# Kernel tuning notes

Hardware: AMD Instinct MI355X
Metric: run time of the kernel (lower is better)

## Reference

```python
import jax, jax.numpy as jnp
import numpy as np

DIM = 256
CTX_DIM = 768
GROUPS = 8
EPS = 1e-5


def setup_inputs() -> dict:
    key = jax.random.key(0)
    ks = jax.random.split(key, 16)
    B, C, H, W, L = 16, DIM, 64, 64, 77
    s_conv = 1.0 / np.sqrt(C * 9)
    s_q = 1.0 / np.sqrt(C)
    s_kv = 1.0 / np.sqrt(CTX_DIM)
    return {
        "x": jax.random.normal(ks[0], (B, C, H, W), jnp.float32),
        "context": jax.random.normal(ks[1], (B, L, CTX_DIM), jnp.float32),
        "conv_w": jax.random.uniform(ks[2], (C, C, 3, 3), jnp.float32, -s_conv, s_conv),
        "conv_b": jax.random.uniform(ks[3], (C,), jnp.float32, -s_conv, s_conv),
        "gn_w": jnp.ones((C,), jnp.float32),
        "gn_b": jnp.zeros((C,), jnp.float32),
        "wq": jax.random.uniform(ks[4], (C, C), jnp.float32, -s_q, s_q),
        "bq": jax.random.uniform(ks[5], (C,), jnp.float32, -s_q, s_q),
        "wk": jax.random.uniform(ks[6], (C, CTX_DIM), jnp.float32, -s_kv, s_kv),
        "bk": jax.random.uniform(ks[7], (C,), jnp.float32, -s_kv, s_kv),
        "wv": jax.random.uniform(ks[8], (C, CTX_DIM), jnp.float32, -s_kv, s_kv),
        "bv": jax.random.uniform(ks[9], (C,), jnp.float32, -s_kv, s_kv),
        "wo": jax.random.uniform(ks[10], (C, C), jnp.float32, -s_q, s_q),
        "bo": jax.random.uniform(ks[11], (C,), jnp.float32, -s_q, s_q),
    }


def _group_norm(h, gn_w, gn_b):
    B, C, H, W = h.shape
    g = h.reshape(B, GROUPS, C // GROUPS, H, W)
    mean = g.mean(axis=(2, 3, 4), keepdims=True)
    var = g.var(axis=(2, 3, 4), keepdims=True)
    g = (g - mean) * jax.lax.rsqrt(var + EPS)
    h = g.reshape(B, C, H, W)
    return h * gn_w[None, :, None, None] + gn_b[None, :, None, None]


def reference(x, context, conv_w, conv_b, gn_w, gn_b, wq, bq, wk, bk, wv, bv, wo, bo):
    B, C, H, W = x.shape
    # conv 3x3, padding=1 (NCHW, OIHW)
    h = jax.lax.conv_general_dilated(
        x, conv_w, window_strides=(1, 1), padding=((1, 1), (1, 1)),
        dimension_numbers=("NCHW", "OIHW", "NCHW"))
    h = h + conv_b[None, :, None, None]
    h = jax.nn.silu(_group_norm(h, gn_w, gn_b))
    # flatten spatial -> tokens: [B, HW, C]
    hf = h.reshape(B, C, H * W).transpose(0, 2, 1)
    q = hf @ wq.T + bq                     # [B, HW, C]
    k = context @ wk.T + bk                # [B, L, C]
    v = context @ wv.T + bv                # [B, L, C]
    scale = 1.0 / jnp.sqrt(jnp.asarray(C, q.dtype))
    att = jax.nn.softmax(jnp.einsum("bqc,bkc->bqk", q, k) * scale, axis=-1)
    o = jnp.einsum("bqk,bkc->bqc", att, v) @ wo.T + bo
    h_att = o.transpose(0, 2, 1).reshape(B, C, H, W)
    return x + h_att
```

## Files before the change

### kernel.cpp

```cpp
#include <hip/hip_runtime.h>
#include <stdint.h>

#define B_  16
#define C_  256
#define HW_ 4096
#define Hp  66
#define PP  4356
#define EPS_ 1e-5f

typedef unsigned short u16;
typedef unsigned int   u32;
typedef __attribute__((ext_vector_type(4))) float  f32x4;
typedef __attribute__((ext_vector_type(8))) __bf16 bf16x8;
typedef __attribute__((ext_vector_type(8))) u16    u16x8;

__device__ __forceinline__ float bf2f(u16 u){ u32 x = ((u32)u)<<16; float f; __builtin_memcpy(&f,&x,4); return f; }
__device__ __forceinline__ u16 f2bf(float f){ u32 x; __builtin_memcpy(&x,&f,4); u32 r = x + 0x7fffu + ((x>>16)&1u); return (u16)(r>>16); }

__device__ __forceinline__ void g2l16(const void* g, void* l){
  __builtin_amdgcn_global_load_lds((__attribute__((address_space(1))) void*)(void*)g,
                                   (__attribute__((address_space(3))) void*)l, 16, 0, 0);
}
__device__ __forceinline__ bf16x8 ldfrag(const u16* p){
  u16x8 r = *(const u16x8*)p;
  return __builtin_bit_cast(bf16x8, r);
}

__global__ __launch_bounds__(256) void k_prep(const float* __restrict__ x, u16* __restrict__ xpT,
    const float* __restrict__ conv_w, const float* __restrict__ wq, const float* __restrict__ wo,
    const float* __restrict__ wk, const float* __restrict__ wv, const float* __restrict__ ctx,
    u16* __restrict__ wBt, u16* __restrict__ wqB, u16* __restrict__ woB,
    u16* __restrict__ wkvB, u16* __restrict__ ctxB, float* __restrict__ stats){
  __shared__ float Lt[64*65];
  int bid = blockIdx.x; int tid = threadIdx.x;
  if(bid >= 1056){
    int i = (bid-1056)*256 + tid;
    if(i < 589824){
      int j = i&7, co = (i>>3)&255, atom = (i>>11)&3, g = i>>13;
      int t = g%9, cic = g/9;
      int ciF = cic*32 + atom*8 + j;
      wBt[i] = f2bf(conv_w[(co*256+ciF)*9 + t]); return;
    }
    i -= 589824;
    if(i < 65536){ wqB[i] = f2bf(wq[i]); return; } i -= 65536;
    if(i < 65536){ woB[i] = f2bf(wo[i]); return; } i -= 65536;
    if(i < 196608){ wkvB[i] = f2bf(wk[i]); return; } i -= 196608;
    if(i < 196608){ wkvB[196608+i] = f2bf(wv[i]); return; } i -= 196608;
    if(i < 946176){ ctxB[i] = f2bf(ctx[i]); return; } i -= 946176;
    if(i < 512){ stats[i] = 0.f; }
    return;
  }
  int b = bid/66, hh = bid - b*66;
  if(hh==0 || hh==65){
    for(int i=tid;i<32*264;i+=256){
      int pl = i/264, off = i - pl*264;
      u32* p = (u32*)(xpT + ((size_t)(b*32+pl)*PP + (size_t)hh*Hp)*8);
      p[off] = 0u;
    }
    return;
  }
  {
    int pl = tid>>3, q = tid&7;
    size_t base = ((size_t)(b*32+pl)*PP + (size_t)hh*Hp + (q>=4?65:0))*8;
    ((u32*)(xpT + base))[q&3] = 0u;
  }
  int h = hh-1;
  for(int cc=0; cc<4; cc++){
    int c0=cc*64;
    int ci = tid>>2, w0 = (tid&3)*16;
    const float* xs = x + ((size_t)(b*C_ + c0+ci)*HW_) + h*64 + w0;
    for(int j=0;j<4;j++){
      float4 v = *(const float4*)(xs + j*4);
      Lt[ci*65 + w0 + j*4 + 0] = v.x;
      Lt[ci*65 + w0 + j*4 + 1] = v.y;
      Lt[ci*65 + w0 + j*4 + 2] = v.z;
      Lt[ci*65 + w0 + j*4 + 3] = v.w;
    }
    __syncthreads();
    int w = tid>>2, cj = (tid&3)*16;
    union { u16 u[16]; uint4 v[2]; } outu;
    for(int j=0;j<16;j++) outu.u[j] = f2bf(Lt[(cj+j)*65 + w]);
    int chan = c0 + cj;
    int cic = chan>>5, at0 = (chan>>3)&3;
    u16* dst = xpT + (((size_t)(b*8+cic)*4 + at0)*PP + (size_t)hh*Hp + w + 1)*8;
    *(uint4*)dst = outu.v[0];
    *(uint4*)(dst + (size_t)PP*8) = outu.v[1];
    __syncthreads();
  }
}

__global__ __launch_bounds__(256, 3) void k_conv(const u16* __restrict__ xpT, const u16* __restrict__ wBt,
    const float* __restrict__ conv_b, u16* __restrict__ h, float* __restrict__ stats){
  __shared__ u16 As[2][264*32];
  __shared__ u16 Bs[2][128*32];
  int bid0 = blockIdx.x;
  int l = (bid0 & 7)*128 + (bid0 >> 3);
  int b = l >> 6, hp = (l >> 1) & 31, nh = l & 1;
  int tid = threadIdx.x;
  int w = tid>>6, lane = tid&63, ln = lane&15, qd = lane>>4;
  int wm = w&1, wn = w>>1;
  f32x4 acc[4][4] = {};
  int hr_[4], wp_[4];
  #pragma unroll
  for(int mf=0;mf<4;mf++){ int p = wm*64 + mf*16 + ln; hr_[mf] = p>>6; wp_[mf] = p&63; }

  #pragma unroll
  for(int r=0;r<5;r++){
    int c = r*256 + tid;
    if(c < 1056){
      int atom = c/264, ipix = c - atom*264;
      g2l16(xpT + (((size_t)(b*8+0)*4 + atom)*PP + hp*132 + ipix)*8, &As[0][c*8]);
    }
  }
  #pragma unroll
  for(int r=0;r<2;r++){
    int c = r*256 + tid;
    int atom = c>>7, col = c&127;
    g2l16(wBt + ((size_t)atom*2048 + (nh*128+col)*8), &Bs[0][c*8]);
  }
  __syncthreads();

  int cb = 0;
  for(int ci=0; ci<8; ci++){
    int ca = ci&1;
    for(int t=0;t<9;t++){
      int tn = t+1, cin = ci;
      if(tn==9){ tn=0; cin=ci+1; }
      if(cin < 8){
        #pragma unroll
        for(int r=0;r<2;r++){
          int c = r*256 + tid;
          int atom = c>>7, col = c&127;
          g2l16(wBt + (((size_t)(cin*9+tn)*4 + atom)*2048 + (nh*128+col)*8), &Bs[cb^1][c*8]);
        }
      }
      if(t<5 && ci<7){
        int c = t*256 + tid;
        if(c < 1056){
          int atom = c/264, ipix = c - atom*264;
          g2l16(xpT + (((size_t)(b*8+ci+1)*4 + atom)*PP + hp*132 + ipix)*8, &As[ca^1][c*8]);
        }
      }
      int dy = (t*11)>>5, dx = t - dy*3;
      bf16x8 af[4], bfv[4];
      #pragma unroll
      for(int mf=0;mf<4;mf++){
        int ipix = (hr_[mf]+dy)*66 + wp_[mf] + dx;
        af[mf] = ldfrag(&As[ca][(qd*264 + ipix)*8]);
      }
      #pragma unroll
      for(int nf=0;nf<4;nf++) bfv[nf] = ldfrag(&Bs[cb][(qd*128 + wn*64+nf*16+ln)*8]);
      #pragma unroll
      for(int mf=0;mf<4;mf++)
        #pragma unroll
        for(int nf=0;nf<4;nf++)
          acc[mf][nf] = __builtin_amdgcn_mfma_f32_16x16x32_bf16(af[mf], bfv[nf], acc[mf][nf], 0,0,0);
      __syncthreads();
      cb ^= 1;
    }
  }
  float s[2]={0,0}, q[2]={0,0};
  int p0 = hp*128;
  for(int nf=0;nf<4;nf++){
    int n = nh*128 + wn*64 + nf*16 + ln;
    float bias = conv_b[n];
    for(int mf=0;mf<4;mf++){
      for(int r=0;r<4;r++){
        int p = wm*64 + mf*16 + qd*4 + r;
        float v = acc[mf][nf][r] + bias;
        h[((size_t)(b*HW_ + p0 + p))*C_ + n] = f2bf(v);
        s[nf>>1]+=v; q[nf>>1]+=v*v;
      }
    }
  }
  for(int off=32;off>=1;off>>=1){
    #pragma unroll
    for(int g=0;g<2;g++){ s[g]+=__shfl_down(s[g],off,64); q[g]+=__shfl_down(q[g],off,64); }
  }
  if(lane==0){
    #pragma unroll
    for(int g=0;g<2;g++){
      int gg = nh*4 + wn*2 + g;
      atomicAdd(&stats[(b*8 + gg)*2+0], s[g]);
      atomicAdd(&stats[(b*8 + gg)*2+1], q[g]);
    }
  }
}

__global__ __launch_bounds__(256, 2) void k_qgn(const u16* __restrict__ hbuf, const u16* __restrict__ wqB,
    const float* __restrict__ stats, const float* __restrict__ gnw, const float* __restrict__ gnb,
    const float* __restrict__ bq, u16* __restrict__ qb){
  __shared__ u16 As[128*32];
  __shared__ u16 Bs[256*32];
  int mt = blockIdx.x;
  int b = mt >> 5;
  int tid = threadIdx.x;
  int w = tid>>6, lane = tid&63, ln = lane&15, qd = lane>>4;
  int wm = w&1, wn = w>>1;
  int pr = tid>>1, half = tid&1;
  const u16* hsrc = hbuf + ((size_t)(mt*128+pr))*256 + half*16;
  f32x4 acc[4][8] = {};
  uint4 ra0, ra1, rb0, rb1;
  ra0 = *(const uint4*)(hsrc);
  ra1 = *(const uint4*)(hsrc + 8);
  for(int kt=0; kt<8; kt++){
    float sm = stats[(b*8+kt)*2], qm = stats[(b*8+kt)*2+1];
    float mean = sm*(1.f/131072.f);
    float rstd = rsqrtf(qm*(1.f/131072.f) - mean*mean + EPS_);
    int c0 = kt*32 + half*16;
    float4 gw0 = *(const float4*)(gnw+c0), gw1 = *(const float4*)(gnw+c0+4);
    float4 gw2 = *(const float4*)(gnw+c0+8), gw3 = *(const float4*)(gnw+c0+12);
    float4 gb0 = *(const float4*)(gnb+c0), gb1 = *(const float4*)(gnb+c0+4);
    float4 gb2 = *(const float4*)(gnb+c0+8), gb3 = *(const float4*)(gnb+c0+12);
    float gwv[16] = {gw0.x,gw0.y,gw0.z,gw0.w, gw1.x,gw1.y,gw1.z,gw1.w,
                     gw2.x,gw2.y,gw2.z,gw2.w, gw3.x,gw3.y,gw3.z,gw3.w};
    float gbv[16] = {gb0.x,gb0.y,gb0.z,gb0.w, gb1.x,gb1.y,gb1.z,gb1.w,
                     gb2.x,gb2.y,gb2.z,gb2.w, gb3.x,gb3.y,gb3.z,gb3.w};
    u16 inu[16];
    ((uint4*)inu)[0] = ra0; ((uint4*)inu)[1] = ra1;
    u16 outu[16];
    #pragma unroll
    for(int j=0;j<16;j++){
      float v = bf2f(inu[j]);
      v = (v-mean)*rstd*gwv[j] + gbv[j];
      float s = v/(1.f+__expf(-v));
      outu[j] = f2bf(s);
    }
    u16* adst = &As[pr*32 + half*16];
    ((uint4*)adst)[0] = ((uint4*)outu)[0];
    ((uint4*)adst)[1] = ((uint4*)outu)[1];
    #pragma unroll
    for(int r=0;r<4;r++){
      int c = r*256 + tid;
      int co = c>>2, atom = c&3;
      g2l16(wqB + (size_t)co*256 + kt*32 + atom*8, &Bs[c*8]);
    }
    if(kt<7){
      rb0 = *(const uint4*)(hsrc + (kt+1)*32);
      rb1 = *(const uint4*)(hsrc + (kt+1)*32 + 8);
    }
    __syncthreads();
    bf16x8 af[4], bfv[8];
    #pragma unroll
    for(int mf=0;mf<4;mf++) af[mf] = ldfrag(&As[(wm*64+mf*16+ln)*32 + qd*8]);
    #pragma unroll
    for(int nf=0;nf<8;nf++) bfv[nf] = ldfrag(&Bs[(wn*128+nf*16+ln)*32 + qd*8]);
    #pragma unroll
    for(int mf=0;mf<4;mf++)
      #pragma unroll
      for(int nf=0;nf<8;nf++)
        acc[mf][nf] = __builtin_amdgcn_mfma_f32_16x16x32_bf16(af[mf], bfv[nf], acc[mf][nf], 0,0,0);
    __syncthreads();
    ra0 = rb0; ra1 = rb1;
  }
  for(int nf=0;nf<8;nf++){
    int n = wn*128 + nf*16 + ln;
    float bias = bq[n];
    for(int mf=0;mf<4;mf++){
      for(int r=0;r<4;r++){
        int ml = wm*64 + mf*16 + qd*4 + r;
        qb[((size_t)(mt*128+ml))*256 + n] = f2bf(acc[mf][nf][r]+bias);
      }
    }
  }
}

__global__ __launch_bounds__(256) void k_kvproj(const u16* __restrict__ ctxB, const u16* __restrict__ wkvB,
    const float* __restrict__ bk, const float* __restrict__ bv,
    u16* __restrict__ kb, u16* __restrict__ vT){
  __shared__ u16 As[64*128];
  __shared__ u16 Bs[64*128];
  int bid = blockIdx.x;
  int nt = bid & 7, mt = bid >> 3;
  int n0 = nt*64, m0 = mt*64;
  int tid=threadIdx.x, w=tid>>6, lane=tid&63, ln=lane&15, qd=lane>>4;
  int wm = w&1, wn = w>>1;
  f32x4 acc[2][2]={};
  for(int kt=0;kt<6;kt++){
    #pragma unroll
    for(int r=0;r<4;r++){
      int c = r*256 + tid;
      int row = c>>4, atom = c&15;
      g2l16(ctxB + ((size_t)(m0+row)*768 + kt*128 + atom*8), &As[c*8]);
      g2l16(wkvB + ((size_t)(n0+row)*768 + kt*128 + atom*8), &Bs[c*8]);
    }
    __syncthreads();
    #pragma unroll
    for(int kk=0;kk<4;kk++){
      bf16x8 af[2], bfv[2];
      #pragma unroll
      for(int mf=0;mf<2;mf++) af[mf]=ldfrag(&As[(wm*32+mf*16+ln)*128 + kk*32 + qd*8]);
      #pragma unroll
      for(int nf=0;nf<2;nf++) bfv[nf]=ldfrag(&Bs[(wn*32+nf*16+ln)*128 + kk*32 + qd*8]);
      #pragma unroll
      for(int mf=0;mf<2;mf++)
        #pragma unroll
        for(int nf=0;nf<2;nf++)
          acc[mf][nf]=__builtin_amdgcn_mfma_f32_16x16x32_bf16(af[mf],bfv[nf],acc[mf][nf],0,0,0);
    }
    __syncthreads();
  }
  for(int mf=0;mf<2;mf++) for(int nf=0;nf<2;nf++){
    int ng = n0 + wn*32 + nf*16 + ln;
    float bias = ng<256 ? bk[ng] : bv[ng-256];
    for(int r=0;r<4;r++){
      int mg = m0 + wm*32 + mf*16 + qd*4 + r;
      if(mg<1232){
        float v=acc[mf][nf][r]+bias;
        int bb=mg/77, l=mg-bb*77;
        if(ng<256) kb[((size_t)(bb*77+l))*256+ng]=f2bf(v);
        else vT[((size_t)(bb*256+(ng-256)))*96 + l]=f2bf(v);
      }
    }
  }
}

__global__ __launch_bounds__(256) void k_attn(const u16* __restrict__ qg, const u16* __restrict__ kb,
    const u16* __restrict__ vT, u16* __restrict__ ob){
  __shared__ u16 Qs[4096];
  __shared__ u16 KVs[4096];
  __shared__ u16 Sb[128*88];
  __shared__ u16 Pb[128*104];
  __shared__ float invr[128];
  int bid=blockIdx.x; int b=bid>>5, qt=bid&31; int p0=qt*128;
  int tid=threadIdx.x, w=tid>>6, lane=tid&63, ln=lane&15, qd=lane>>4;
  int srow=tid>>2, koff=(tid&3)*8;
  f32x4 Sa[2][5]={};
  for(int kt=0;kt<8;kt++){
    for(int j=0;j<2;j++){
      int m=srow+j*64;
      g2l16(qg + ((size_t)(b*HW_+p0+m)*256 + kt*32+koff), &Qs[(size_t)tid*8+j*2048]);
    }
    for(int j=0;j<2;j++){
      int cja = tid + j*256;
      if(cja < 320){
        int l = cja>>2, ko2=(cja&3)*8;
        g2l16(kb + ((size_t)(b*77+l)*256 + kt*32+ko2), &KVs[(size_t)cja*8]);
      }
    }
    __syncthreads();
    bf16x8 af[2], bfv[5];
    for(int mf=0;mf<2;mf++) af[mf]=ldfrag(&Qs[(w*32+mf*16+ln)*32+qd*8]);
    for(int nf=0;nf<5;nf++) bfv[nf]=ldfrag(&KVs[(nf*16+ln)*32+qd*8]);
    for(int mf=0;mf<2;mf++) for(int nf=0;nf<5;nf++)
      Sa[mf][nf]=__builtin_amdgcn_mfma_f32_16x16x32_bf16(af[mf],bfv[nf],Sa[mf][nf],0,0,0);
    __syncthreads();
  }
  for(int mf=0;mf<2;mf++) for(int nf=0;nf<5;nf++) for(int r=0;r<4;r++){
    int ml=w*32+mf*16+qd*4+r, nl=nf*16+ln;
    Sb[ml*88+nl]=f2bf(Sa[mf][nf][r]*0.0625f);
  }
  __syncthreads();
  if(tid<128){
    u16* srp = &Sb[tid*88];
    srp[77]=0xFF80u; srp[78]=0xFF80u; srp[79]=0xFF80u;
    float mx=-1e30f;
    #pragma unroll
    for(int c8=0;c8<10;c8++){
      u16x8 v = *(const u16x8*)(srp + c8*8);
      #pragma unroll
      for(int j=0;j<8;j++) mx = fmaxf(mx, bf2f(v[j]));
    }
    u16* prow = &Pb[tid*104];
    float sum=0.f;
    #pragma unroll
    for(int c8=0;c8<10;c8++){
      u16x8 v = *(const u16x8*)(srp + c8*8);
      u16x8 o;
      #pragma unroll
      for(int j=0;j<8;j++){ float e=__expf(bf2f(v[j])-mx); sum+=e; o[j]=f2bf(e); }
      *(u16x8*)(prow + c8*8) = o;
    }
    #pragma unroll
    for(int j=80;j<96;j++) prow[j]=0;
    invr[tid] = 1.f/sum;
  }
  __syncthreads();
  for(int nh=0;nh<2;nh++){
    f32x4 Oa[2][8]={};
    for(int kt2=0;kt2<3;kt2++){
      for(int j=0;j<2;j++){
        int chunk=tid+j*256;
        int co=chunk>>2, ko2=(chunk&3)*8;
        g2l16(vT + ((size_t)(b*256+nh*128+co)*96 + kt2*32+ko2), &KVs[(size_t)chunk*8]);
      }
      __syncthreads();
      bf16x8 af[2], bfv[8];
      for(int mf=0;mf<2;mf++) af[mf]=ldfrag(&Pb[(w*32+mf*16+ln)*104 + kt2*32+qd*8]);
      for(int nf=0;nf<8;nf++) bfv[nf]=ldfrag(&KVs[(nf*16+ln)*32+qd*8]);
      for(int mf=0;mf<2;mf++) for(int nf=0;nf<8;nf++)
        Oa[mf][nf]=__builtin_amdgcn_mfma_f32_16x16x32_bf16(af[mf],bfv[nf],Oa[mf][nf],0,0,0);
      __syncthreads();
    }
    for(int mf=0;mf<2;mf++){
      #pragma unroll
      for(int r=0;r<4;r++){
        int ml=w*32+mf*16+qd*4+r;
        float inv = invr[ml];
        for(int nf=0;nf<8;nf++){
          int nl=nh*128+nf*16+ln;
          ob[((size_t)(b*HW_+p0+ml))*256+nl]=f2bf(Oa[mf][nf][r]*inv);
        }
      }
    }
  }
}

__global__ __launch_bounds__(256) void k_oproj(const u16* __restrict__ ob, const u16* __restrict__ woB,
    const float* __restrict__ bo, const float* __restrict__ x, float* __restrict__ outp){
  __shared__ u16 As[128*32];
  __shared__ u16 Bs[128*32];
  int bid=blockIdx.x;
  int b=bid>>6; int rr=bid&63; int cm=rr>>5, pt=rr&31;
  int c0=cm*128, p0=pt*128;
  int tid=threadIdx.x, w=tid>>6, lane=tid&63, ln=lane&15, qd=lane>>4, wm=w>>1, wn=w&1;
  int srow=tid>>2, koff=(tid&3)*8;
  f32x4 acc[4][4]={};
  for(int kt=0;kt<8;kt++){
    for(int j=0;j<2;j++){
      int m=srow+j*64;
      g2l16(woB + ((size_t)(c0+m)*256 + kt*32+koff),        &As[(size_t)tid*8+j*2048]);
      g2l16(ob  + ((size_t)(b*HW_+p0+m)*256 + kt*32+koff),  &Bs[(size_t)tid*8+j*2048]);
    }
    __syncthreads();
    bf16x8 af[4], bfv[4];
    for(int mf=0;mf<4;mf++) af[mf]=ldfrag(&As[(wm*64+mf*16+ln)*32+qd*8]);
    for(int nf=0;nf<4;nf++) bfv[nf]=ldfrag(&Bs[(wn*64+nf*16+ln)*32+qd*8]);
    for(int mf=0;mf<4;mf++) for(int nf=0;nf<4;nf++)
      acc[mf][nf]=__builtin_amdgcn_mfma_f32_16x16x32_bf16(af[mf],bfv[nf],acc[mf][nf],0,0,0);
    __syncthreads();
  }
  for(int mf=0;mf<4;mf++) for(int r=0;r<4;r++){
    int cl=c0+wm*64+mf*16+qd*4+r;
    float bias=bo[cl];
    for(int nf=0;nf<4;nf++){
      int pl=p0+wn*64+nf*16+ln;
      size_t idx=((size_t)(b*C_+cl))*HW_+pl;
      outp[idx]=x[idx]+acc[mf][nf][r]+bias;
    }
  }
}

extern "C" void kernel_launch(void* const* d_in, const int* in_sizes, int n_in,
                              void* d_out, int out_size, void* d_ws, size_t ws_size,
                              hipStream_t stream){
  const float* x      = (const float*)d_in[0];
  const float* ctx    = (const float*)d_in[1];
  const float* conv_w = (const float*)d_in[2];
  const float* conv_b = (const float*)d_in[3];
  const float* gnw    = (const float*)d_in[4];
  const float* gnb    = (const float*)d_in[5];
  const float* wq     = (const float*)d_in[6];
  const float* bq     = (const float*)d_in[7];
  const float* wk     = (const float*)d_in[8];
  const float* bk     = (const float*)d_in[9];
  const float* wv     = (const float*)d_in[10];
  const float* bv     = (const float*)d_in[11];
  const float* wo     = (const float*)d_in[12];
  const float* bo     = (const float*)d_in[13];
  char* ws = (char*)d_ws;
  u16* xpT  = (u16*)(ws + 0);
  u16* wBt  = (u16*)(ws + 35684352);
  u16* wqB  = (u16*)(ws + 36864000);
  u16* wkvB = (u16*)(ws + 36995072);
  u16* woB  = (u16*)(ws + 37781504);
  u16* ctxB = (u16*)(ws + 37912576);
  u16* hbuf = (u16*)(ws + 39804928);
  u16* kbv  = (u16*)(ws + 73359360);
  u16* vT   = (u16*)(ws + 73990144);
  u16* obuf = (u16*)(ws + 74776576);
  float* stats = (float*)(ws + 108331008);
  u16* qb = xpT;
  float* outp = (float*)d_out;

  k_prep  <<<9106, 256, 0, stream>>>(x, xpT, conv_w, wq, wo, wk, wv, ctx, wBt, wqB, woB, wkvB, ctxB, stats);
  k_conv  <<<1024, 256, 0, stream>>>(xpT, wBt, conv_b, hbuf, stats);
  k_qgn   <<<512,  256, 0, stream>>>(hbuf, wqB, stats, gnw, gnb, bq, qb);
  k_kvproj<<<160,  256, 0, stream>>>(ctxB, wkvB, bk, bv, kbv, vT);
  k_attn  <<<512,  256, 0, stream>>>(qb, kbv, vT, obuf);
  k_oproj <<<1024, 256, 0, stream>>>(obuf, woB, bo, x, outp);
}
```

Baseline: 380.0 us.

## Restructure attention kernel: preload full K/V to LDS, register-resident softmax

The attention kernel now loads the whole K tile (and later the whole V^T tile) into LDS in one batch instead of in per-k-step chunks, and loads the Q fragments straight from global memory into registers. This removes most of the per-iteration __syncthreads. Softmax now runs on the MFMA accumulators in registers, using wave shuffles for the row max and sum, rather than staging scores through a bf16 LDS buffer with a single-thread-per-row loop. Launch bounds request 2 blocks per CU. The costs are higher register pressure from holding Q fragments in registers and a larger LDS footprint (about 48KB for KVf).

```diff
diff --git a/kernel.cpp b/kernel.cpp
--- a/kernel.cpp
+++ b/kernel.cpp
@@ -315,88 +315,134 @@
   }
 }
 
-__global__ __launch_bounds__(256) void k_attn(const u16* __restrict__ qg, const u16* __restrict__ kb,
+__global__ __launch_bounds__(256, 2) void k_attn(const u16* __restrict__ qg, const u16* __restrict__ kb,
     const u16* __restrict__ vT, u16* __restrict__ ob){
-  __shared__ u16 Qs[4096];
-  __shared__ u16 KVs[4096];
-  __shared__ u16 Sb[128*88];
+  __shared__ u16 KVf[3072*8];
   __shared__ u16 Pb[128*104];
   __shared__ float invr[128];
   int bid=blockIdx.x; int b=bid>>5, qt=bid&31; int p0=qt*128;
   int tid=threadIdx.x, w=tid>>6, lane=tid&63, ln=lane&15, qd=lane>>4;
-  int srow=tid>>2, koff=(tid&3)*8;
+
+  #pragma unroll
+  for(int j=0;j<10;j++){
+    int c = tid + j*256;
+    int kt = c/320, rem = c - kt*320;
+    int q2 = rem/80, l = rem - q2*80;
+    int ls = l<77 ? l : 76;
+    g2l16(kb + ((size_t)(b*77+ls)*256 + kt*32 + q2*8), &KVf[(size_t)c*8]);
+  }
+  bf16x8 qf[2][8];
+  #pragma unroll
+  for(int mf=0;mf<2;mf++){
+    const u16* qsrc = qg + ((size_t)(b*HW_ + p0 + w*32 + mf*16 + ln))*256 + qd*8;
+    #pragma unroll
+    for(int kt=0;kt<8;kt++) qf[mf][kt] = ldfrag(qsrc + kt*32);
+  }
+  __syncthreads();
+
   f32x4 Sa[2][5]={};
+  #pragma unroll
   for(int kt=0;kt<8;kt++){
-    for(int j=0;j<2;j++){
-      int m=srow+j*64;
-      g2l16(qg + ((size_t)(b*HW_+p0+m)*256 + kt*32+koff), &Qs[(size_t)tid*8+j*2048]);
-    }
-    for(int j=0;j<2;j++){
-      int cja = tid + j*256;
-      if(cja < 320){
-        int l = cja>>2, ko2=(cja&3)*8;
-        g2l16(kb + ((size_t)(b*77+l)*256 + kt*32+ko2), &KVs[(size_t)cja*8]);
-      }
-    }
-    __syncthreads();
-    bf16x8 af[2], bfv[5];
-    for(int mf=0;mf<2;mf++) af[mf]=ldfrag(&Qs[(w*32+mf*16+ln)*32+qd*8]);
-    for(int nf=0;nf<5;nf++) bfv[nf]=ldfrag(&KVs[(nf*16+ln)*32+qd*8]);
-    for(int mf=0;mf<2;mf++) for(int nf=0;nf<5;nf++)
-      Sa[mf][nf]=__builtin_amdgcn_mfma_f32_16x16x32_bf16(af[mf],bfv[nf],Sa[mf][nf],0,0,0);
-    __syncthreads();
-  }
-  for(int mf=0;mf<2;mf++) for(int nf=0;nf<5;nf++) for(int r=0;r<4;r++){
-    int ml=w*32+mf*16+qd*4+r, nl=nf*16+ln;
-    Sb[ml*88+nl]=f2bf(Sa[mf][nf][r]*0.0625f);
+    bf16x8 kf[5];
+    #pragma unroll
+    for(int nf=0;nf<5;nf++) kf[nf]=ldfrag(&KVf[((size_t)kt*320 + qd*80 + nf*16+ln)*8]);
+    #pragma unroll
+    for(int mf=0;mf<2;mf++)
+      #pragma unroll
+      for(int nf=0;nf<5;nf++)
+        Sa[mf][nf]=__builtin_amdgcn_mfma_f32_16x16x32_bf16(qf[mf][kt],kf[nf],Sa[mf][nf],0,0,0);
+  }
+  if(ln>=13){
+    #pragma unroll
+    for(int mf=0;mf<2;mf++)
+      #pragma unroll
+      for(int r=0;r<4;r++) Sa[mf][4][r] = -1e30f;
+  }
+  float mrow[2][4];
+  #pragma unroll
+  for(int mf=0;mf<2;mf++)
+    #pragma unroll
+    for(int r=0;r<4;r++){
+      float m = Sa[mf][0][r];
+      #pragma unroll
+      for(int nf=1;nf<5;nf++) m = fmaxf(m, Sa[mf][nf][r]);
+      mrow[mf][r]=m;
+    }
+  #pragma unroll
+  for(int off=1;off<16;off<<=1)
+    #pragma unroll
+    for(int mf=0;mf<2;mf++)
+      #pragma unroll
+      for(int r=0;r<4;r++) mrow[mf][r] = fmaxf(mrow[mf][r], __shfl_xor(mrow[mf][r], off, 64));
+  float rs[2][4]={};
+  u16 pe[2][5][4];
+  #pragma unroll
+  for(int mf=0;mf<2;mf++)
+    #pragma unroll
+    for(int nf=0;nf<5;nf++)
+      #pragma unroll
+      for(int r=0;r<4;r++){
+        float e = __expf((Sa[mf][nf][r]-mrow[mf][r])*0.0625f);
+        rs[mf][r]+=e; pe[mf][nf][r]=f2bf(e);
+      }
+  #pragma unroll
+  for(int off=1;off<16;off<<=1)
+    #pragma unroll
+    for(int mf=0;mf<2;mf++)
+      #pragma unroll
+      for(int r=0;r<4;r++) rs[mf][r] += __shfl_xor(rs[mf][r], off, 64);
+  #pragma unroll
+  for(int mf=0;mf<2;mf++)
+    #pragma unroll
+    for(int nf=0;nf<5;nf++)
+      #pragma unroll
+      for(int r=0;r<4;r++) Pb[(w*32+mf*16+qd*4+r)*104 + nf*16+ln] = pe[mf][nf][r];
+  {
+    int row = tid>>1, j0 = (tid&1)*8;
+    u16x8 z = {0,0,0,0,0,0,0,0};
+    *(u16x8*)&Pb[row*104 + 80 + j0] = z;
+  }
+  if(ln==0){
+    #pragma unroll
+    for(int mf=0;mf<2;mf++)
+      #pragma unroll
+      for(int r=0;r<4;r++) invr[w*32+mf*16+qd*4+r] = 1.f/rs[mf][r];
   }
   __syncthreads();
-  if(tid<128){
-    u16* srp = &Sb[tid*88];
-    srp[77]=0xFF80u; srp[78]=0xFF80u; srp[79]=0xFF80u;
-    float mx=-1e30f;
-    #pragma unroll
-    for(int c8=0;c8<10;c8++){
-      u16x8 v = *(const u16x8*)(srp + c8*8);
-      #pragma unroll
-      for(int j=0;j<8;j++) mx = fmaxf(mx, bf2f(v[j]));
-    }
-    u16* prow = &Pb[tid*104];
-    float sum=0.f;
-    #pragma unroll
-    for(int c8=0;c8<10;c8++){
-      u16x8 v = *(const u16x8*)(srp + c8*8);
-      u16x8 o;
-      #pragma unroll
-      for(int j=0;j<8;j++){ float e=__expf(bf2f(v[j])-mx); sum+=e; o[j]=f2bf(e); }
-      *(u16x8*)(prow + c8*8) = o;
-    }
-    #pragma unroll
-    for(int j=80;j<96;j++) prow[j]=0;
-    invr[tid] = 1.f/sum;
+
+  #pragma unroll
+  for(int j=0;j<12;j++){
+    int c = tid + j*256;
+    int g = c>>7, co = c&127;
+    int q2 = g&3, s5 = g>>2;
+    int nh2 = s5>2 ? 1 : 0, kt2 = s5 - 3*nh2;
+    g2l16(vT + ((size_t)(b*256 + nh2*128 + co)*96 + kt2*32 + q2*8), &KVf[(size_t)c*8]);
   }
   __syncthreads();
+
+  #pragma unroll
   for(int nh=0;nh<2;nh++){
     f32x4 Oa[2][8]={};
+    #pragma unroll
     for(int kt2=0;kt2<3;kt2++){
-      for(int j=0;j<2;j++){
-        int chunk=tid+j*256;
-        int co=chunk>>2, ko2=(chunk&3)*8;
-        g2l16(vT + ((size_t)(b*256+nh*128+co)*96 + kt2*32+ko2), &KVs[(size_t)chunk*8]);
-      }
-      __syncthreads();
-      bf16x8 af[2], bfv[8];
-      for(int mf=0;mf<2;mf++) af[mf]=ldfrag(&Pb[(w*32+mf*16+ln)*104 + kt2*32+qd*8]);
-      for(int nf=0;nf<8;nf++) bfv[nf]=ldfrag(&KVs[(nf*16+ln)*32+qd*8]);
-      for(int mf=0;mf<2;mf++) for(int nf=0;nf<8;nf++)
-        Oa[mf][nf]=__builtin_amdgcn_mfma_f32_16x16x32_bf16(af[mf],bfv[nf],Oa[mf][nf],0,0,0);
-      __syncthreads();
-    }
+      bf16x8 pa[2], vf[8];
+      #pragma unroll
+      for(int mf=0;mf<2;mf++) pa[mf]=ldfrag(&Pb[(w*32+mf*16+ln)*104 + kt2*32+qd*8]);
+      #pragma unroll
+      for(int nf=0;nf<8;nf++) vf[nf]=ldfrag(&KVf[(((size_t)(nh*3+kt2)*4+qd)*128 + nf*16+ln)*8]);
+      #pragma unroll
+      for(int mf=0;mf<2;mf++)
+        #pragma unroll
+        for(int nf=0;nf<8;nf++)
+          Oa[mf][nf]=__builtin_amdgcn_mfma_f32_16x16x32_bf16(pa[mf],vf[nf],Oa[mf][nf],0,0,0);
+    }
+    #pragma unroll
     for(int mf=0;mf<2;mf++){
       #pragma unroll
       for(int r=0;r<4;r++){
         int ml=w*32+mf*16+qd*4+r;
         float inv = invr[ml];
+        #pragma unroll
         for(int nf=0;nf<8;nf++){
           int nl=nh*128+nf*16+ln;
           ob[((size_t)(b*HW_+p0+ml))*256+nl]=f2bf(Oa[mf][nf][r]*inv);
```

Measured after the change: 366.3 us. 3.6% less time.
